# Kernel optimization log

Measured on AMD Instinct MI355X. Metric: run time of the kernel, lower is better.

Reference implementation:

```python
import jax, jax.numpy as jnp
import numpy as np

N = 50000      # nodes
E = 200000     # edges per edge type (avg in-degree 16 over 4 etypes)
R = 4          # number of edge types
DIN = 128
DH = 128
DOUT = 64


def setup_inputs() -> dict:
    key = jax.random.key(0)
    ks = jax.random.split(key, 6)
    feat = jax.random.normal(ks[0], (N, DIN), dtype=jnp.float32)
    edges = jax.random.randint(ks[1], (R, 2, E), 0, N)  # [R, (src,dst), E]
    s1 = 1.0 / np.sqrt(DIN)
    W1 = jax.random.uniform(ks[2], (R, DIN, DH), jnp.float32, -s1, s1)
    b1 = jax.random.uniform(ks[3], (R, DH), jnp.float32, -s1, s1)
    s2 = 1.0 / np.sqrt(DH)
    W2 = jax.random.uniform(ks[4], (R, DH, DOUT), jnp.float32, -s2, s2)
    b2 = jax.random.uniform(ks[5], (R, DOUT), jnp.float32, -s2, s2)
    return {"feat": feat, "W1": W1, "b1": b1, "W2": W2, "b2": b2, "edges": edges}


def _hetero_layer(h, W, b, edges):
    """Per-etype Linear -> copy_u + mean over in-edges -> sum across etypes."""
    n = h.shape[0]

    def per_etype(Wr, br, er):
        Wh = h @ Wr + br                       # [N, d_out]
        src, dst = er[0], er[1]
        msg = Wh[src]                          # gather [E, d_out]
        ssum = jax.ops.segment_sum(msg, dst, num_segments=n)
        deg = jax.ops.segment_sum(jnp.ones((er.shape[1],), Wh.dtype), dst,
                                  num_segments=n)
        return ssum / jnp.maximum(deg, 1.0)[:, None]   # mean; 0 for isolated nodes

    return jax.vmap(per_etype)(W, b, edges).sum(axis=0)  # 'sum' cross reducer


def reference(feat, W1, b1, W2, b2, edges):
    h = _hetero_layer(feat, W1, b1, edges)
    h = jax.nn.relu(h)
    return _hetero_layer(h, W2, b2, edges)
```

## Files before the change

kernel.cpp:

```cpp
#include <hip/hip_runtime.h>

#define NN 50000
#define EE 200000
#define RR 4
#define SC_TOTAL (RR * NN)
#define CAP 32
#define GTILE ((NN + 127) / 128)

typedef __attribute__((ext_vector_type(8))) short bf16x8;
typedef __attribute__((ext_vector_type(4))) float f32x4;

__device__ inline unsigned short f2bf(float x) {
    unsigned int u = __float_as_uint(x);
    u += 0x7fffu + ((u >> 16) & 1u);
    return (unsigned short)(u >> 16);
}
__device__ inline float bflo(unsigned u) { return __uint_as_float(u << 16); }
__device__ inline float bfhi(unsigned u) { return __uint_as_float(u & 0xffff0000u); }

__global__ __launch_bounds__(256) void init_kernel(
    const float* __restrict__ feat, unsigned short* __restrict__ featb,
    const float* __restrict__ W1, const float* __restrict__ b1,
    const float* __restrict__ W2, const float* __restrict__ b2,
    unsigned short* __restrict__ W1T, unsigned short* __restrict__ W2T,
    float* __restrict__ btab1, float* __restrict__ btab2,
    int* __restrict__ cnt)
{
    int b = blockIdx.x, t = threadIdx.x;
    if (b < 6250) {
        int i = (b * 256 + t) * 4;
        float4 v = *(const float4*)&feat[i];
        unsigned lo = (unsigned)f2bf(v.x) | ((unsigned)f2bf(v.y) << 16);
        unsigned hi = (unsigned)f2bf(v.z) | ((unsigned)f2bf(v.w) << 16);
        *(uint2*)&featb[i] = make_uint2(lo, hi);
    } else if (b < 6506) {
        int i = (b - 6250) * 256 + t;
        int jout = i >> 7, k = i & 127;
        int r = jout >> 7, j = jout & 127;
        W1T[i] = f2bf(W1[r * 16384 + k * 128 + j]);
    } else if (b < 6634) {
        int i = (b - 6506) * 256 + t;
        int jout = i >> 7, k = i & 127;
        int r = jout >> 6, j = jout & 63;
        W2T[i] = f2bf(W2[r * 8192 + k * 64 + j]);
    } else if (b < 6642) {
        int i = (b - 6634) * 256 + t;
        int mm = i >> 7, c = i & 127;
        float s = 0.f;
        #pragma unroll
        for (int r = 0; r < RR; ++r) if (mm & (1 << r)) s += b1[r * 128 + c];
        btab1[i] = s;
    } else if (b < 6646) {
        int i = (b - 6642) * 256 + t;
        int mm = i >> 6, c = i & 63;
        float s = 0.f;
        #pragma unroll
        for (int r = 0; r < RR; ++r) if (mm & (1 << r)) s += b2[r * 64 + c];
        btab2[i] = s;
    } else {
        int i = ((b - 6646) * 256 + t) * 4;
        if (i < SC_TOTAL * 16) *(int4*)&cnt[i] = make_int4(0, 0, 0, 0);
    }
}

__global__ __launch_bounds__(256) void fill_append(
    const int* __restrict__ edges, int* __restrict__ cnt,
    unsigned short* __restrict__ ssrc2)
{
    int r = blockIdx.y;
    int e = blockIdx.x * 256 + threadIdx.x;
    if (e >= EE) return;
    const int* es = edges + (size_t)r * 2 * EE;
    int src = es[e];
    int dst = es[EE + e];
    int seg = r * NN + dst;
    int p = atomicAdd(&cnt[seg * 16], 1);
    if (p < CAP) ssrc2[(size_t)seg * CAP + p] = (unsigned short)src;
}

template<int OTOT>
__global__ __launch_bounds__(256) void gemm_tf(
    const unsigned short* __restrict__ A, const unsigned short* __restrict__ WT,
    unsigned short* __restrict__ H)
{
    __shared__ __align__(16) unsigned short Wl[128 * 128];
    const int tid  = threadIdx.x;
    const int wv   = tid >> 6;
    const int lane = tid & 63;
    const int m    = lane & 15;
    const int q    = lane >> 4;
    const int col0 = blockIdx.x * 128;
    const int row0 = blockIdx.y * 128;

    #pragma unroll
    for (int i = 0; i < 8; ++i) {
        int L  = i * 4096 + tid * 16;
        int nr = L >> 8, ir = L & 255;
        uint4 v = *(const uint4*)((const char*)WT + ((size_t)(col0 + nr) << 8) + ir);
        *(uint4*)((char*)Wl + nr * 256 + (ir ^ ((nr & 7) << 4))) = v;
    }
    __syncthreads();

    f32x4 acc[2][8];
    #pragma unroll
    for (int rf = 0; rf < 2; ++rf)
        #pragma unroll
        for (int nt = 0; nt < 8; ++nt) acc[rf][nt] = (f32x4){0.f, 0.f, 0.f, 0.f};

    const int ra0 = row0 + wv * 32 + m;
    const int ra1 = ra0 + 16;
    const bool g0 = ra0 < NN, g1 = ra1 < NN;
    const unsigned short* Ap0 = A + (size_t)ra0 * 128 + q * 8;
    const unsigned short* Ap1 = A + (size_t)ra1 * 128 + q * 8;
    const bf16x8 bz = (bf16x8){0, 0, 0, 0, 0, 0, 0, 0};

    #pragma unroll
    for (int kk = 0; kk < 4; ++kk) {
        bf16x8 a0 = g0 ? *(const bf16x8*)(Ap0 + kk * 32) : bz;
        bf16x8 a1 = g1 ? *(const bf16x8*)(Ap1 + kk * 32) : bz;
        #pragma unroll
        for (int nt = 0; nt < 8; ++nt) {
            int offb = (nt * 16 + m) * 256 + ((kk * 64 + q * 16) ^ ((m & 7) << 4));
            bf16x8 bfr = *(const bf16x8*)((const char*)Wl + offb);
            acc[0][nt] = __builtin_amdgcn_mfma_f32_16x16x32_bf16(a0, bfr, acc[0][nt], 0, 0, 0);
            acc[1][nt] = __builtin_amdgcn_mfma_f32_16x16x32_bf16(a1, bfr, acc[1][nt], 0, 0, 0);
        }
    }

    #pragma unroll
    for (int rf = 0; rf < 2; ++rf) {
        #pragma unroll
        for (int rg = 0; rg < 4; ++rg) {
            int row = row0 + wv * 32 + rf * 16 + q * 4 + rg;
            if (row < NN) {
                unsigned short* Hp = H + (size_t)row * OTOT + col0 + m;
                #pragma unroll
                for (int nt = 0; nt < 8; ++nt)
                    Hp[nt * 16] = f2bf(acc[rf][nt][rg]);
            }
        }
    }
}

__global__ __launch_bounds__(256) void gather_node1(
    const unsigned short* __restrict__ H1, const unsigned short* __restrict__ ssrc2,
    const int* __restrict__ cnt, const float* __restrict__ btab1,
    unsigned short* __restrict__ h1r)
{
    int n = blockIdx.x * 16 + (threadIdx.x >> 4);
    if (n >= NN) return;
    int l = threadIdx.x & 15;
    float a0 = 0.f, a1 = 0.f, a2 = 0.f, a3 = 0.f, a4 = 0.f, a5 = 0.f, a6 = 0.f, a7 = 0.f;
    int mk = 0;
    #pragma unroll
    for (int r = 0; r < RR; ++r) {
        int seg = r * NN + n;
        int deg = cnt[seg * 16];
        if (deg <= 0) continue;
        mk |= 1 << r;
        const unsigned short* lst  = ssrc2 + (size_t)seg * CAP;
        const unsigned short* base = H1 + r * 128 + l * 8;
        float b0 = 0.f, b1v = 0.f, b2v = 0.f, b3 = 0.f, b4 = 0.f, b5 = 0.f, b6 = 0.f, b7 = 0.f;
        int j = 0;
        for (; j + 1 < deg; j += 2) {
            uint4 u0 = *(const uint4*)(base + (size_t)lst[j] * 512);
            uint4 u1 = *(const uint4*)(base + (size_t)lst[j + 1] * 512);
            b0 += bflo(u0.x) + bflo(u1.x); b1v += bfhi(u0.x) + bfhi(u1.x);
            b2v += bflo(u0.y) + bflo(u1.y); b3 += bfhi(u0.y) + bfhi(u1.y);
            b4 += bflo(u0.z) + bflo(u1.z); b5 += bfhi(u0.z) + bfhi(u1.z);
            b6 += bflo(u0.w) + bflo(u1.w); b7 += bfhi(u0.w) + bfhi(u1.w);
        }
        if (j < deg) {
            uint4 u0 = *(const uint4*)(base + (size_t)lst[j] * 512);
            b0 += bflo(u0.x); b1v += bfhi(u0.x);
            b2v += bflo(u0.y); b3 += bfhi(u0.y);
            b4 += bflo(u0.z); b5 += bfhi(u0.z);
            b6 += bflo(u0.w); b7 += bfhi(u0.w);
        }
        float inv = 1.0f / (float)deg;
        a0 += b0 * inv; a1 += b1v * inv; a2 += b2v * inv; a3 += b3 * inv;
        a4 += b4 * inv; a5 += b5 * inv; a6 += b6 * inv; a7 += b7 * inv;
    }
    const float* bt = btab1 + mk * 128 + l * 8;
    float4 t0 = *(const float4*)bt;
    float4 t1 = *(const float4*)(bt + 4);
    uint4 o;
    o.x = (unsigned)f2bf(fmaxf(a0 + t0.x, 0.f)) | ((unsigned)f2bf(fmaxf(a1 + t0.y, 0.f)) << 16);
    o.y = (unsigned)f2bf(fmaxf(a2 + t0.z, 0.f)) | ((unsigned)f2bf(fmaxf(a3 + t0.w, 0.f)) << 16);
    o.z = (unsigned)f2bf(fmaxf(a4 + t1.x, 0.f)) | ((unsigned)f2bf(fmaxf(a5 + t1.y, 0.f)) << 16);
    o.w = (unsigned)f2bf(fmaxf(a6 + t1.z, 0.f)) | ((unsigned)f2bf(fmaxf(a7 + t1.w, 0.f)) << 16);
    *(uint4*)&h1r[(size_t)n * 128 + l * 8] = o;
}

__global__ __launch_bounds__(256) void gather_node2(
    const unsigned short* __restrict__ H2, const unsigned short* __restrict__ ssrc2,
    const int* __restrict__ cnt, const float* __restrict__ btab2,
    float* __restrict__ out)
{
    int n = blockIdx.x * 32 + (threadIdx.x >> 3);
    if (n >= NN) return;
    int l = threadIdx.x & 7;
    float a0 = 0.f, a1 = 0.f, a2 = 0.f, a3 = 0.f, a4 = 0.f, a5 = 0.f, a6 = 0.f, a7 = 0.f;
    int mk = 0;
    #pragma unroll
    for (int r = 0; r < RR; ++r) {
        int seg = r * NN + n;
        int deg = cnt[seg * 16];
        if (deg <= 0) continue;
        mk |= 1 << r;
        const unsigned short* lst  = ssrc2 + (size_t)seg * CAP;
        const unsigned short* base = H2 + r * 64 + l * 8;
        float b0 = 0.f, b1v = 0.f, b2v = 0.f, b3 = 0.f, b4 = 0.f, b5 = 0.f, b6 = 0.f, b7 = 0.f;
        int j = 0;
        for (; j + 1 < deg; j += 2) {
            uint4 u0 = *(const uint4*)(base + (size_t)lst[j] * 256);
            uint4 u1 = *(const uint4*)(base + (size_t)lst[j + 1] * 256);
            b0 += bflo(u0.x) + bflo(u1.x); b1v += bfhi(u0.x) + bfhi(u1.x);
            b2v += bflo(u0.y) + bflo(u1.y); b3 += bfhi(u0.y) + bfhi(u1.y);
            b4 += bflo(u0.z) + bflo(u1.z); b5 += bfhi(u0.z) + bfhi(u1.z);
            b6 += bflo(u0.w) + bflo(u1.w); b7 += bfhi(u0.w) + bfhi(u1.w);
        }
        if (j < deg) {
            uint4 u0 = *(const uint4*)(base + (size_t)lst[j] * 256);
            b0 += bflo(u0.x); b1v += bfhi(u0.x);
            b2v += bflo(u0.y); b3 += bfhi(u0.y);
            b4 += bflo(u0.z); b5 += bfhi(u0.z);
            b6 += bflo(u0.w); b7 += bfhi(u0.w);
        }
        float inv = 1.0f / (float)deg;
        a0 += b0 * inv; a1 += b1v * inv; a2 += b2v * inv; a3 += b3 * inv;
        a4 += b4 * inv; a5 += b5 * inv; a6 += b6 * inv; a7 += b7 * inv;
    }
    const float* bt = btab2 + mk * 64 + l * 8;
    float4 t0 = *(const float4*)bt;
    float4 t1 = *(const float4*)(bt + 4);
    float* op = out + (size_t)n * 64 + l * 8;
    *(float4*)op       = make_float4(a0 + t0.x, a1 + t0.y, a2 + t0.z, a3 + t0.w);
    *(float4*)(op + 4) = make_float4(a4 + t1.x, a5 + t1.y, a6 + t1.z, a7 + t1.w);
}

extern "C" void kernel_launch(void* const* d_in, const int* in_sizes, int n_in,
                              void* d_out, int out_size, void* d_ws, size_t ws_size,
                              hipStream_t stream)
{
    const float* feat  = (const float*)d_in[0];
    const float* W1    = (const float*)d_in[1];
    const float* b1    = (const float*)d_in[2];
    const float* W2    = (const float*)d_in[3];
    const float* b2    = (const float*)d_in[4];
    const int*   edges = (const int*)d_in[5];
    float* out = (float*)d_out;

    char* p = (char*)d_ws;
    auto alloc = [&](size_t bytes) { char* q = p; p += (bytes + 255) & ~(size_t)255; return q; };
    int* cnt                 = (int*)alloc((size_t)SC_TOTAL * 16 * 4);
    unsigned short* ssrc2    = (unsigned short*)alloc((size_t)SC_TOTAL * CAP * 2);
    unsigned short* W1T      = (unsigned short*)alloc((size_t)512 * 128 * 2);
    unsigned short* W2T      = (unsigned short*)alloc((size_t)256 * 128 * 2);
    float* btab1             = (float*)alloc((size_t)16 * 128 * 4);
    float* btab2             = (float*)alloc((size_t)16 * 64 * 4);
    unsigned short* featb    = (unsigned short*)alloc((size_t)NN * 128 * 2);
    unsigned short* h1r      = (unsigned short*)alloc((size_t)NN * 128 * 2);
    unsigned short* H        = (unsigned short*)alloc((size_t)NN * 512 * 2);

    init_kernel<<<9771, 256, 0, stream>>>(feat, featb, W1, b1, W2, b2,
                                          W1T, W2T, btab1, btab2, cnt);
    dim3 fg((EE + 255) / 256, RR);
    fill_append<<<fg, 256, 0, stream>>>(edges, cnt, ssrc2);

    gemm_tf<512><<<dim3(4, GTILE), 256, 0, stream>>>(featb, W1T, H);
    gather_node1<<<(NN + 15) / 16, 256, 0, stream>>>(H, ssrc2, cnt, btab1, h1r);
    gemm_tf<256><<<dim3(2, GTILE), 256, 0, stream>>>(h1r, W2T, H);
    gather_node2<<<(NN + 31) / 32, 256, 0, stream>>>(H, ssrc2, cnt, btab2, out);
}
```

Before: 228.5 us.

## Fuse edge-list fill into first GEMM launch and compact degree counters

```diff
diff --git a/kernel.cpp b/kernel.cpp
--- a/kernel.cpp
+++ b/kernel.cpp
@@ -6,6 +6,8 @@
 #define SC_TOTAL (RR * NN)
 #define CAP 32
 #define GTILE ((NN + 127) / 128)
+#define NB_G1 (4 * GTILE)
+#define NB_F  1563
 
 typedef __attribute__((ext_vector_type(8))) short bf16x8;
 typedef __attribute__((ext_vector_type(4))) float f32x4;
@@ -59,23 +61,95 @@
         btab2[i] = s;
     } else {
         int i = ((b - 6646) * 256 + t) * 4;
-        if (i < SC_TOTAL * 16) *(int4*)&cnt[i] = make_int4(0, 0, 0, 0);
-    }
-}
-
-__global__ __launch_bounds__(256) void fill_append(
+        if (i < SC_TOTAL) *(int4*)&cnt[i] = make_int4(0, 0, 0, 0);
+    }
+}
+
+__global__ __launch_bounds__(256) void fill_gemm1(
     const int* __restrict__ edges, int* __restrict__ cnt,
-    unsigned short* __restrict__ ssrc2)
-{
-    int r = blockIdx.y;
-    int e = blockIdx.x * 256 + threadIdx.x;
-    if (e >= EE) return;
-    const int* es = edges + (size_t)r * 2 * EE;
-    int src = es[e];
-    int dst = es[EE + e];
-    int seg = r * NN + dst;
-    int p = atomicAdd(&cnt[seg * 16], 1);
-    if (p < CAP) ssrc2[(size_t)seg * CAP + p] = (unsigned short)src;
+    unsigned short* __restrict__ ssrc2,
+    const unsigned short* __restrict__ A, const unsigned short* __restrict__ WT,
+    unsigned short* __restrict__ H)
+{
+    __shared__ __align__(16) unsigned short Wl[128 * 128];
+    const int bid = blockIdx.x;
+    const int tid = threadIdx.x;
+
+    if (bid & 1) {
+        int f = bid >> 1;
+        #pragma unroll
+        for (int k = 0; k < 2; ++k) {
+            int i = f * 512 + k * 256 + tid;
+            if (i < RR * EE) {
+                int r = i / EE;
+                int e = i - r * EE;
+                const int* es = edges + (size_t)r * 2 * EE;
+                int src = es[e];
+                int dst = es[EE + e];
+                int seg = r * NN + dst;
+                int p = atomicAdd(&cnt[seg], 1);
+                if (p < CAP) ssrc2[(size_t)seg * CAP + p] = (unsigned short)src;
+            }
+        }
+        return;
+    }
+
+    const int g    = bid >> 1;
+    const int wv   = tid >> 6;
+    const int lane = tid & 63;
+    const int m    = lane & 15;
+    const int q    = lane >> 4;
+    const int col0 = (g & 3) * 128;
+    const int row0 = (g >> 2) * 128;
+
+    #pragma unroll
+    for (int i = 0; i < 8; ++i) {
+        int L  = i * 4096 + tid * 16;
+        int nr = L >> 8, ir = L & 255;
+        uint4 v = *(const uint4*)((const char*)WT + ((size_t)(col0 + nr) << 8) + ir);
+        *(uint4*)((char*)Wl + nr * 256 + (ir ^ ((nr & 7) << 4))) = v;
+    }
+    __syncthreads();
+
+    f32x4 acc[2][8];
+    #pragma unroll
+    for (int rf = 0; rf < 2; ++rf)
+        #pragma unroll
+        for (int nt = 0; nt < 8; ++nt) acc[rf][nt] = (f32x4){0.f, 0.f, 0.f, 0.f};
+
+    const int ra0 = row0 + wv * 32 + m;
+    const int ra1 = ra0 + 16;
+    const bool g0 = ra0 < NN, g1 = ra1 < NN;
+    const unsigned short* Ap0 = A + (size_t)ra0 * 128 + q * 8;
+    const unsigned short* Ap1 = A + (size_t)ra1 * 128 + q * 8;
+    const bf16x8 bz = (bf16x8){0, 0, 0, 0, 0, 0, 0, 0};
+
+    #pragma unroll
+    for (int kk = 0; kk < 4; ++kk) {
+        bf16x8 a0 = g0 ? *(const bf16x8*)(Ap0 + kk * 32) : bz;
+        bf16x8 a1 = g1 ? *(const bf16x8*)(Ap1 + kk * 32) : bz;
+        #pragma unroll
+        for (int nt = 0; nt < 8; ++nt) {
+            int offb = (nt * 16 + m) * 256 + ((kk * 64 + q * 16) ^ ((m & 7) << 4));
+            bf16x8 bfr = *(const bf16x8*)((const char*)Wl + offb);
+            acc[0][nt] = __builtin_amdgcn_mfma_f32_16x16x32_bf16(a0, bfr, acc[0][nt], 0, 0, 0);
+            acc[1][nt] = __builtin_amdgcn_mfma_f32_16x16x32_bf16(a1, bfr, acc[1][nt], 0, 0, 0);
+        }
+    }
+
+    #pragma unroll
+    for (int rf = 0; rf < 2; ++rf) {
+        #pragma unroll
+        for (int rg = 0; rg < 4; ++rg) {
+            int row = row0 + wv * 32 + rf * 16 + q * 4 + rg;
+            if (row < NN) {
+                unsigned short* Hp = H + (size_t)row * 512 + col0 + m;
+                #pragma unroll
+                for (int nt = 0; nt < 8; ++nt)
+                    Hp[nt * 16] = f2bf(acc[rf][nt][rg]);
+            }
+        }
+    }
 }
 
 template<int OTOT>
@@ -155,14 +229,15 @@
     #pragma unroll
     for (int r = 0; r < RR; ++r) {
         int seg = r * NN + n;
-        int deg = cnt[seg * 16];
+        int deg = cnt[seg];
         if (deg <= 0) continue;
         mk |= 1 << r;
+        int nd = (deg < CAP) ? deg : CAP;
         const unsigned short* lst  = ssrc2 + (size_t)seg * CAP;
         const unsigned short* base = H1 + r * 128 + l * 8;
         float b0 = 0.f, b1v = 0.f, b2v = 0.f, b3 = 0.f, b4 = 0.f, b5 = 0.f, b6 = 0.f, b7 = 0.f;
         int j = 0;
-        for (; j + 1 < deg; j += 2) {
+        for (; j + 1 < nd; j += 2) {
             uint4 u0 = *(const uint4*)(base + (size_t)lst[j] * 512);
             uint4 u1 = *(const uint4*)(base + (size_t)lst[j + 1] * 512);
             b0 += bflo(u0.x) + bflo(u1.x); b1v += bfhi(u0.x) + bfhi(u1.x);
@@ -170,7 +245,7 @@
             b4 += bflo(u0.z) + bflo(u1.z); b5 += bfhi(u0.z) + bfhi(u1.z);
             b6 += bflo(u0.w) + bflo(u1.w); b7 += bfhi(u0.w) + bfhi(u1.w);
         }
-        if (j < deg) {
+        if (j < nd) {
             uint4 u0 = *(const uint4*)(base + (size_t)lst[j] * 512);
             b0 += bflo(u0.x); b1v += bfhi(u0.x);
             b2v += bflo(u0.y); b3 += bfhi(u0.y);
@@ -205,14 +280,15 @@
     #pragma unroll
     for (int r = 0; r < RR; ++r) {
         int seg = r * NN + n;
-        int deg = cnt[seg * 16];
+        int deg = cnt[seg];
         if (deg <= 0) continue;
         mk |= 1 << r;
+        int nd = (deg < CAP) ? deg : CAP;
         const unsigned short* lst  = ssrc2 + (size_t)seg * CAP;
         const unsigned short* base = H2 + r * 64 + l * 8;
         float b0 = 0.f, b1v = 0.f, b2v = 0.f, b3 = 0.f, b4 = 0.f, b5 = 0.f, b6 = 0.f, b7 = 0.f;
         int j = 0;
-        for (; j + 1 < deg; j += 2) {
+        for (; j + 1 < nd; j += 2) {
             uint4 u0 = *(const uint4*)(base + (size_t)lst[j] * 256);
             uint4 u1 = *(const uint4*)(base + (size_t)lst[j + 1] * 256);
             b0 += bflo(u0.x) + bflo(u1.x); b1v += bfhi(u0.x) + bfhi(u1.x);
@@ -220,7 +296,7 @@
             b4 += bflo(u0.z) + bflo(u1.z); b5 += bfhi(u0.z) + bfhi(u1.z);
             b6 += bflo(u0.w) + bflo(u1.w); b7 += bfhi(u0.w) + bfhi(u1.w);
         }
-        if (j < deg) {
+        if (j < nd) {
             uint4 u0 = *(const uint4*)(base + (size_t)lst[j] * 256);
             b0 += bflo(u0.x); b1v += bfhi(u0.x);
             b2v += bflo(u0.y); b3 += bfhi(u0.y);
@@ -253,7 +329,7 @@
 
     char* p = (char*)d_ws;
     auto alloc = [&](size_t bytes) { char* q = p; p += (bytes + 255) & ~(size_t)255; return q; };
-    int* cnt                 = (int*)alloc((size_t)SC_TOTAL * 16 * 4);
+    int* cnt                 = (int*)alloc((size_t)SC_TOTAL * 4);
     unsigned short* ssrc2    = (unsigned short*)alloc((size_t)SC_TOTAL * CAP * 2);
     unsigned short* W1T      = (unsigned short*)alloc((size_t)512 * 128 * 2);
     unsigned short* W2T      = (unsigned short*)alloc((size_t)256 * 128 * 2);
@@ -263,12 +339,9 @@
     unsigned short* h1r      = (unsigned short*)alloc((size_t)NN * 128 * 2);
     unsigned short* H        = (unsigned short*)alloc((size_t)NN * 512 * 2);
 
-    init_kernel<<<9771, 256, 0, stream>>>(feat, featb, W1, b1, W2, b2,
+    init_kernel<<<6842, 256, 0, stream>>>(feat, featb, W1, b1, W2, b2,
                                           W1T, W2T, btab1, btab2, cnt);
-    dim3 fg((EE + 255) / 256, RR);
-    fill_append<<<fg, 256, 0, stream>>>(edges, cnt, ssrc2);
-
-    gemm_tf<512><<<dim3(4, GTILE), 256, 0, stream>>>(featb, W1T, H);
+    fill_gemm1<<<NB_G1 + NB_F, 256, 0, stream>>>(edges, cnt, ssrc2, featb, W1T, H);
     gather_node1<<<(NN + 15) / 16, 256, 0, stream>>>(H, ssrc2, cnt, btab1, h1r);
     gemm_tf<256><<<dim3(2, GTILE), 256, 0, stream>>>(h1r, W2T, H);
     gather_node2<<<(NN + 31) / 32, 256, 0, stream>>>(H, ssrc2, cnt, btab2, out);
```

Measured after the change: 200.2 us. 1.14x faster.
